# Optimization experiments

Hardware: AMD Instinct MI355X
Metric: run time of the kernel (lower is better)

## Reference

```python
import jax, jax.numpy as jnp
import numpy as np

NH = 4
TEMP = 0.5

def _ln(x, w, b):
    mu = x.mean(-1, keepdims=True)
    var = ((x - mu) ** 2).mean(-1, keepdims=True)
    return (x - mu) / jnp.sqrt(var + 1e-5) * w + b

def _encoder(x, bias, key_pad, layers):
    # pre-LN torch TransformerEncoder, relu FFN, dropout=0
    Wqkv, bqkv, Wo, bo, ln1w, ln1b, ln2w, ln2b, W1, b1, W2, b2 = layers
    B, L, H = x.shape
    d = H // NH
    scale = 1.0 / np.sqrt(d)
    for i in range(Wqkv.shape[0]):
        y = _ln(x, ln1w[i], ln1b[i])
        qkv = y @ Wqkv[i].T + bqkv[i]
        q, k, v = jnp.split(qkv, 3, axis=-1)
        q = q.reshape(B, L, NH, d).transpose(0, 2, 1, 3)
        k = k.reshape(B, L, NH, d).transpose(0, 2, 1, 3)
        v = v.reshape(B, L, NH, d).transpose(0, 2, 1, 3)
        s = jnp.einsum('bhqd,bhkd->bhqk', q, k) * scale
        if bias is not None:
            s = s + bias
        s = s + key_pad[:, None, None, :]
        a = jax.nn.softmax(s, axis=-1)
        o = jnp.einsum('bhqk,bhkd->bhqd', a, v).transpose(0, 2, 1, 3).reshape(B, L, H)
        x = x + o @ Wo[i].T + bo[i]
        y = _ln(x, ln2w[i], ln2b[i])
        x = x + jax.nn.relu(y @ W1[i].T + b1[i]) @ W2[i].T + b2[i]
    return x

def _layer_params(key, nl, H, F, sc=0.05):
    ks = jax.random.split(key, 4)
    return (jax.random.normal(ks[0], (nl, 3 * H, H)) * sc, jnp.zeros((nl, 3 * H)),
            jax.random.normal(ks[1], (nl, H, H)) * sc, jnp.zeros((nl, H)),
            jnp.ones((nl, H)), jnp.zeros((nl, H)), jnp.ones((nl, H)), jnp.zeros((nl, H)),
            jax.random.normal(ks[2], (nl, F, H)) * sc, jnp.zeros((nl, F)),
            jax.random.normal(ks[3], (nl, H, F)) * sc, jnp.zeros((nl, H)))

def setup_inputs():
    key = jax.random.key(0)
    IN, H, ED, F = 64, 128, 16, 256
    G, NPG = 8, 512
    N = G * NPG
    m, k = 4, 16
    T = N
    S = T * m
    EPS = 24
    E_loc = S * EPS
    E = 65536
    ks = jax.random.split(key, 13)
    x = jax.random.normal(ks[0], (N, IN))
    log_probs = -jnp.abs(jax.random.normal(ks[1], (S,)))
    root = jnp.repeat(jnp.arange(T), m)
    base = (root // NPG) * NPG
    rest = base[:, None] + jax.random.randint(ks[2], (S, k - 1), 0, NPG)
    nodes_sampled = jnp.concatenate([root[:, None], rest], axis=1)
    valid = jnp.ones((S * k,), dtype=bool)
    edge_index_sampled = jax.random.randint(ks[3], (2, E_loc), 0, k)
    edge_ptr = jnp.arange(S + 1) * EPS
    ea_flat = jax.random.normal(ks[4], (E_loc, ED))
    src = jax.random.randint(ks[5], (E,), 0, N)
    dst = (src // NPG) * NPG + jax.random.randint(ks[6], (E,), 0, NPG)
    edge_index = jnp.stack([src, dst])
    edge_attr = jax.random.normal(ks[7], (E, ED))
    batch_vec = jnp.arange(N) // NPG
    ptr = jnp.arange(G + 1) * NPG
    d = dict(x=x, log_probs=log_probs, ea_flat=ea_flat, edge_attr=edge_attr,
             init_W=jax.random.normal(ks[8], (H, IN + 2)) * 0.05, init_b=jnp.zeros((H,)),
             loc_ep_W=jax.random.normal(ks[9], (NH, ED)) * 0.05, loc_ep_b=jnp.zeros((NH,)),
             glob_ep_W=jax.random.normal(ks[10], (NH, ED)) * 0.05, glob_ep_b=jnp.zeros((NH,)),
             loc_nw=jnp.ones((H,)), loc_nb=jnp.zeros((H,)),
             glob_nw=jnp.ones((H,)), glob_nb=jnp.zeros((H,)),
             nodes_sampled=nodes_sampled, edge_index_sampled=edge_index_sampled,
             edge_ptr=edge_ptr, edge_index=edge_index, batch_vec=batch_vec,
             ptr=ptr, valid=valid)
    names = ['Wqkv', 'bqkv', 'Wo', 'bo', 'ln1w', 'ln1b', 'ln2w', 'ln2b', 'W1', 'b1', 'W2', 'b2']
    for n, a in zip(names, _layer_params(ks[11], 4, H, F)):
        d['loc_' + n] = a
    for n, a in zip(names, _layer_params(ks[12], 4, H, F)):
        d['glob_' + n] = a
    return d

def reference(x, log_probs, ea_flat, edge_attr, init_W, init_b, loc_ep_W, loc_ep_b,
              glob_ep_W, glob_ep_b, loc_nw, loc_nb, glob_nw, glob_nb,
              loc_Wqkv, loc_bqkv, loc_Wo, loc_bo, loc_ln1w, loc_ln1b, loc_ln2w, loc_ln2b,
              loc_W1, loc_b1, loc_W2, loc_b2,
              glob_Wqkv, glob_bqkv, glob_Wo, glob_bo, glob_ln1w, glob_ln1b, glob_ln2w, glob_ln2b,
              glob_W1, glob_b1, glob_W2, glob_b2,
              nodes_sampled, edge_index_sampled, edge_ptr, edge_index, batch_vec, ptr, valid):
    S, k = nodes_sampled.shape
    N = x.shape[0]
    T = N
    m = S // T
    G = ptr.shape[0] - 1
    max_N = N // G  # equal-size graphs
    H = init_W.shape[0]
    # ---- phase 1: flatten subgraphs + init features ----
    x_flat = x[nodes_sampled.reshape(-1)]                         # [S*k, IN]
    root_global = jnp.repeat(jnp.arange(T), m)                    # [S]
    root_local = jnp.argmax(nodes_sampled == root_global[:, None], axis=1)
    root_mask = jnp.zeros((S * k,), x.dtype).at[jnp.arange(S) * k + root_local].set(1.0)
    lp = jnp.where(jnp.isfinite(log_probs), log_probs, 0.0)
    lp_flat = jnp.repeat(lp, k)[:, None] * valid[:, None].astype(x.dtype)
    h = jnp.concatenate([x_flat, lp_flat, root_mask[:, None]], axis=1) @ init_W.T + init_b
    # ---- local edge bias (scatter-add) ----
    E_loc = ea_flat.shape[0]
    sub = jnp.searchsorted(edge_ptr, jnp.arange(E_loc), side='right') - 1
    eap = ea_flat @ loc_ep_W.T + loc_ep_b                         # [E_loc, NH]
    lbias = jnp.zeros((S, k, k, NH), x.dtype).at[sub, edge_index_sampled[0], edge_index_sampled[1]].add(eap).transpose(0, 3, 1, 2)
    v2 = valid.reshape(S, k)
    key_pad_l = jnp.where(v2, 0.0, -1e9).astype(x.dtype)
    loc_layers = (loc_Wqkv, loc_bqkv, loc_Wo, loc_bo, loc_ln1w, loc_ln1b, loc_ln2w, loc_ln2b, loc_W1, loc_b1, loc_W2, loc_b2)
    out = _encoder(h.reshape(S, k, H), lbias, key_pad_l, loc_layers)
    out = _ln(out, loc_nw, loc_nb)
    vf = v2.astype(x.dtype)[..., None]
    sub_embs = (out * vf).sum(1) / jnp.maximum(vf.sum(1), 1.0)    # [S, H]
    # ---- weighted-mean aggregation over m samples per target node ----
    w = jax.nn.softmax(log_probs.reshape(T, m) / TEMP, axis=1)
    node_embs = jnp.einsum('tm,tmh->th', w, sub_embs.reshape(T, m, H))
    # ---- global phase: to_dense_batch + edge-bias transformer ----
    pos = jnp.arange(N) - ptr[batch_vec]
    dense = jnp.zeros((G, max_N, H), x.dtype).at[batch_vec, pos].set(node_embs)
    vmask = jnp.zeros((G, max_N), bool).at[batch_vec, pos].set(True)
    g = batch_vec[edge_index[0]]
    sl = edge_index[0] - ptr[g]
    dl = edge_index[1] - ptr[g]
    eag = edge_attr @ glob_ep_W.T + glob_ep_b
    gbias = jnp.zeros((G, max_N, max_N, NH), x.dtype).at[g, sl, dl].add(eag).transpose(0, 3, 1, 2)
    key_pad_g = jnp.where(vmask, 0.0, -1e9).astype(x.dtype)
    glob_layers = (glob_Wqkv, glob_bqkv, glob_Wo, glob_bo, glob_ln1w, glob_ln1b, glob_ln2w, glob_ln2b, glob_W1, glob_b1, glob_W2, glob_b2)
    gout = _encoder(dense, gbias, key_pad_g, glob_layers)
    gout = _ln(gout, glob_nw, glob_nb)
    return (gout * vmask[..., None].astype(x.dtype)).sum(1)      # [G, H]
```

## Files before the change

kernel.cpp:

```cpp
#include <hip/hip_runtime.h>
#include <math.h>

#define IN_F      64
#define H_DIM     128
#define NH_       4
#define DH_       32
#define FF_DIM    256
#define KSUB      16
#define S_SEQ     16384
#define E_LOC     393216
#define G_NUM     8
#define NPG_      512
#define N_NODES   4096
#define E_GLOB    65536
#define NLAYERS   4
#define SCALE_ATT 0.17677669529663687f

#define WQKV_SZ   (3*H_DIM*H_DIM)
#define WO_SZ     (H_DIM*H_DIM)
#define W1_SZ     (FF_DIM*H_DIM)
#define W2_SZ     (H_DIM*FF_DIM)

#define ATT(sg)   (4352 + (sg) * 2560)
#define PS_OFF    9472
#define STG_SZ    10112

typedef __bf16 bf16x8 __attribute__((ext_vector_type(8)));
typedef float  f32x4  __attribute__((ext_vector_type(4)));

__device__ __forceinline__ unsigned short f2bf(float f) {
    unsigned u = __float_as_uint(f);
    unsigned r = (u + 0x7fffu + ((u >> 16) & 1u)) >> 16;
    return (unsigned short)r;
}

__device__ __forceinline__ f32x4 mfma16(bf16x8 a, bf16x8 b, f32x4 c) {
    return __builtin_amdgcn_mfma_f32_16x16x32_bf16(a, b, c, 0, 0, 0);
}

__device__ __forceinline__ void ln_to_row(const float (&X)[8][4],
    const float* __restrict__ w, const float* __restrict__ b,
    unsigned short* rowb, int r, int q)
{
    float s1[4] = {0,0,0,0}, s2[4] = {0,0,0,0};
    #pragma unroll
    for (int t = 0; t < 8; ++t)
        #pragma unroll
        for (int i = 0; i < 4; ++i) { float v = X[t][i]; s1[i] += v; s2[i] += v*v; }
    #pragma unroll
    for (int i = 0; i < 4; ++i) {
        float a = s1[i], c = s2[i];
        a += __shfl_xor(a, 1, 16); a += __shfl_xor(a, 2, 16);
        a += __shfl_xor(a, 4, 16); a += __shfl_xor(a, 8, 16);
        c += __shfl_xor(c, 1, 16); c += __shfl_xor(c, 2, 16);
        c += __shfl_xor(c, 4, 16); c += __shfl_xor(c, 8, 16);
        float mu = a * (1.f / H_DIM);
        float var = c * (1.f / H_DIM) - mu * mu;
        s1[i] = mu; s2[i] = rsqrtf(fmaxf(var, 0.f) + 1e-5f);
    }
    for (int t = 0; t < 8; ++t) {
        float wv = w[t * 16 + r], bv = b[t * 16 + r];
        #pragma unroll
        for (int i = 0; i < 4; ++i)
            rowb[(q * 4 + i) * 136 + t * 16 + r] = f2bf((X[t][i] - s1[i]) * s2[i] * wv + bv);
    }
}

__device__ __forceinline__ void ln_mean_out(const float (&X)[8][4],
    const float* __restrict__ fnw, const float* __restrict__ fnb,
    float* __restrict__ dst, int r, int q)
{
    float s1[4] = {0,0,0,0}, s2[4] = {0,0,0,0};
    #pragma unroll
    for (int t = 0; t < 8; ++t)
        #pragma unroll
        for (int i = 0; i < 4; ++i) { float v = X[t][i]; s1[i] += v; s2[i] += v*v; }
    #pragma unroll
    for (int i = 0; i < 4; ++i) {
        float a = s1[i], c = s2[i];
        a += __shfl_xor(a, 1, 16); a += __shfl_xor(a, 2, 16);
        a += __shfl_xor(a, 4, 16); a += __shfl_xor(a, 8, 16);
        c += __shfl_xor(c, 1, 16); c += __shfl_xor(c, 2, 16);
        c += __shfl_xor(c, 4, 16); c += __shfl_xor(c, 8, 16);
        float mu = a * (1.f / H_DIM);
        float var = c * (1.f / H_DIM) - mu * mu;
        s1[i] = mu; s2[i] = rsqrtf(fmaxf(var, 0.f) + 1e-5f);
    }
    float colsum[8];
    #pragma unroll
    for (int t = 0; t < 8; ++t) {
        float wv = fnw[t * 16 + r], bv = fnb[t * 16 + r];
        float cs = 0.f;
        #pragma unroll
        for (int i = 0; i < 4; ++i) cs += (X[t][i] - s1[i]) * s2[i] * wv + bv;
        cs += __shfl_xor(cs, 16, 64);
        cs += __shfl_xor(cs, 32, 64);
        colsum[t] = cs;
    }
    float c0 = (q == 0) ? colsum[0] : (q == 1) ? colsum[1] : (q == 2) ? colsum[2] : colsum[3];
    float c1 = (q == 0) ? colsum[4] : (q == 1) ? colsum[5] : (q == 2) ? colsum[6] : colsum[7];
    dst[q * 16 + r]       = c0 * (1.f / KSUB);
    dst[(q + 4) * 16 + r] = c1 * (1.f / KSUB);
}

__global__ __launch_bounds__(256) void conv_all_k(
    const float* __restrict__ lWqkv, const float* __restrict__ lWo,
    const float* __restrict__ lW1, const float* __restrict__ lW2,
    const float* __restrict__ x,
    const float* __restrict__ gWqkv, const float* __restrict__ gWo,
    const float* __restrict__ gW1, const float* __restrict__ gW2,
    const float* __restrict__ init_W,
    unsigned short* __restrict__ wq_b, unsigned short* __restrict__ wo_b,
    unsigned short* __restrict__ w1_b, unsigned short* __restrict__ w2_b,
    unsigned short* __restrict__ x_b,
    unsigned short* __restrict__ gwq_b, unsigned short* __restrict__ gwo_b,
    unsigned short* __restrict__ gw1_b, unsigned short* __restrict__ gw2_b,
    unsigned short* __restrict__ wi_b)
{
    int b = blockIdx.x, t = threadIdx.x;
    const float* src; unsigned short* dst; int base;
    if (b < 768)       { src = lWqkv; dst = wq_b;  base = b; }
    else if (b < 1024) { src = lWo;   dst = wo_b;  base = b - 768; }
    else if (b < 1536) { src = lW1;   dst = w1_b;  base = b - 1024; }
    else if (b < 2048) { src = lW2;   dst = w2_b;  base = b - 1536; }
    else if (b < 3072) { src = x;     dst = x_b;   base = b - 2048; }
    else if (b < 3840) { src = gWqkv; dst = gwq_b; base = b - 3072; }
    else if (b < 4096) { src = gWo;   dst = gwo_b; base = b - 3840; }
    else if (b < 4608) { src = gW1;   dst = gw1_b; base = b - 4096; }
    else if (b < 5120) { src = gW2;   dst = gw2_b; base = b - 4608; }
    else {
        int i = (b - 5120) * 256 + t;
        int row = i >> 6, c = i & 63;
        wi_b[i] = f2bf(init_W[row * 66 + c]);
        return;
    }
    int i = base * 256 + t;
    dst[i] = f2bf(src[i]);
}

__global__ __launch_bounds__(64) void local_encoder_k(
    const unsigned short* __restrict__ xb16,
    const float* __restrict__ log_probs,
    const float* __restrict__ ea_flat,
    const float* __restrict__ init_W,
    const float* __restrict__ init_b,
    const unsigned short* __restrict__ wi_b,
    const float* __restrict__ ep_W, const float* __restrict__ ep_b,
    const int* __restrict__ nodes, const int* __restrict__ eis,
    const unsigned short* __restrict__ wqb, const unsigned short* __restrict__ wob,
    const unsigned short* __restrict__ w1b, const unsigned short* __restrict__ w2b,
    const float* __restrict__ bqkv, const float* __restrict__ bo,
    const float* __restrict__ ln1w, const float* __restrict__ ln1b,
    const float* __restrict__ ln2w, const float* __restrict__ ln2b,
    const float* __restrict__ b1, const float* __restrict__ b2,
    const float* __restrict__ fnw, const float* __restrict__ fnb,
    float* __restrict__ sub_embs)
{
    __shared__ unsigned short stg[STG_SZ];

    const int lane = threadIdx.x & 63;
    const int r = lane & 15, q = lane >> 4;
    const int s0 = blockIdx.x * 2;
    float* biasWrk = (float*)(stg + 4352);

    {
        float2 z2f; z2f.x = 0.f; z2f.y = 0.f;
        for (int i = lane; i < 1024; i += 64) ((float2*)biasWrk)[i] = z2f;
    }

    int ndA = nodes[s0 * KSUB + r];
    int ndB = nodes[(s0 + 1) * KSUB + r];
    int rootA = s0 >> 2, rootB = (s0 + 1) >> 2;
    unsigned long long balA = __ballot((q == 0) && (ndA == rootA));
    unsigned long long balB = __ballot((q == 0) && (ndB == rootB));
    int rjA = balA ? (__ffsll((long long)balA) - 1) : 0;
    int rjB = balB ? (__ffsll((long long)balB) - 1) : 0;
    float lpA = log_probs[s0];     if (!isfinite(lpA)) lpA = 0.f;
    float lpB = log_probs[s0 + 1]; if (!isfinite(lpB)) lpB = 0.f;

    if (lane < 48) {
        int ls = lane / 24, ee = lane % 24;
        int e = (s0 + ls) * 24 + ee;
        int i0 = eis[e], i1 = eis[E_LOC + e];
        const float* ea = ea_flat + (size_t)e * 16;
        float4 e0 = *(const float4*)(ea), e1 = *(const float4*)(ea + 4);
        float4 e2 = *(const float4*)(ea + 8), e3 = *(const float4*)(ea + 12);
        #pragma unroll
        for (int h = 0; h < NH_; ++h) {
            const float* wp = ep_W + h * 16;
            float v = ep_b[h]
                + e0.x * wp[0]  + e0.y * wp[1]  + e0.z * wp[2]  + e0.w * wp[3]
                + e1.x * wp[4]  + e1.y * wp[5]  + e1.z * wp[6]  + e1.w * wp[7]
                + e2.x * wp[8]  + e2.y * wp[9]  + e2.z * wp[10] + e2.w * wp[11]
                + e3.x * wp[12] + e3.y * wp[13] + e3.z * wp[14] + e3.w * wp[15];
            atomicAdd(&biasWrk[ls * 1024 + (h * 16 + i0) * 16 + i1], v);
        }
    }

    for (int i2 = lane; i2 < 256; i2 += 64) {
        int sg = i2 >> 7, row = (i2 >> 3) & 15, seg = i2 & 7;
        int nd = __shfl(sg ? ndB : ndA, row, 64);
        *(uint4*)(stg + sg * 2176 + row * 136 + seg * 8) =
            *(const uint4*)(xb16 + (size_t)nd * IN_F + seg * 8);
    }

    float bT[2][NH_][4];
    #pragma unroll
    for (int sg = 0; sg < 2; ++sg)
        #pragma unroll
        for (int h = 0; h < NH_; ++h)
            #pragma unroll
            for (int i = 0; i < 4; ++i)
                bT[sg][h][i] = biasWrk[sg * 1024 + (h * 16 + q * 4 + i) * 16 + r];

    {
        uint2 z2; z2.x = 0; z2.y = 0;
        for (int i = lane; i < 320; i += 64) ((uint2*)(stg + ATT(0) + 1280))[i] = z2;
        for (int i = lane; i < 320; i += 64) ((uint2*)(stg + ATT(1) + 1280))[i] = z2;
    }

    float X[2][8][4];
    {
        bf16x8 aA0 = *(const bf16x8*)(stg + r * 136 + q * 8);
        bf16x8 aA1 = *(const bf16x8*)(stg + r * 136 + 32 + q * 8);
        bf16x8 aB0 = *(const bf16x8*)(stg + 2176 + r * 136 + q * 8);
        bf16x8 aB1 = *(const bf16x8*)(stg + 2176 + r * 136 + 32 + q * 8);
        const unsigned short* wr0 = wi_b + (size_t)r * 64 + q * 8;
        bf16x8 c0 = *(const bf16x8*)(wr0);
        bf16x8 c1 = *(const bf16x8*)(wr0 + 32);
        for (int t = 0; t < 8; ++t) {
            bf16x8 n0, n1;
            if (t < 7) {
                const unsigned short* wn = wr0 + (t + 1) * 1024;
                n0 = *(const bf16x8*)(wn);
                n1 = *(const bf16x8*)(wn + 32);
            }
            f32x4 accA = {0.f,0.f,0.f,0.f}, accB = {0.f,0.f,0.f,0.f};
            accA = mfma16(aA0, c0, accA); accA = mfma16(aA1, c1, accA);
            accB = mfma16(aB0, c0, accB); accB = mfma16(aB1, c1, accB);
            int o = t * 16 + r;
            float w64 = init_W[o * 66 + 64], w65 = init_W[o * 66 + 65], bb = init_b[o];
            #pragma unroll
            for (int i = 0; i < 4; ++i) {
                float vA = accA[i] + lpA * w64 + bb;
                float vB = accB[i] + lpB * w64 + bb;
                if (q * 4 + i == rjA) vA += w65;
                if (q * 4 + i == rjB) vB += w65;
                X[0][t][i] = vA; X[1][t][i] = vB;
            }
            c0 = n0; c1 = n1;
        }
    }

    for (int l = 0; l < NLAYERS; ++l) {
        const unsigned short* wq_l = wqb + (size_t)l * WQKV_SZ;
        const unsigned short* wo_l = wob + (size_t)l * WO_SZ;
        const unsigned short* w1_l = w1b + (size_t)l * W1_SZ;
        const unsigned short* w2_l = w2b + (size_t)l * W2_SZ;

        ln_to_row(X[0], ln1w + l * H_DIM, ln1b + l * H_DIM, stg, r, q);
        ln_to_row(X[1], ln1w + l * H_DIM, ln1b + l * H_DIM, stg + 2176, r, q);
        bf16x8 af[2][4];
        #pragma unroll
        for (int sg = 0; sg < 2; ++sg)
            #pragma unroll
            for (int kt = 0; kt < 4; ++kt)
                af[sg][kt] = *(const bf16x8*)(stg + sg * 2176 + r * 136 + kt * 32 + q * 8);

        for (int h = 0; h < NH_; ++h) {
            #pragma unroll
            for (int t = 0; t < 2; ++t) {
                #pragma unroll
                for (int p = 0; p < 3; ++p) {
                    const unsigned short* wr =
                        wq_l + (size_t)(p * H_DIM + h * DH_ + t * 16 + r) * H_DIM + q * 8;
                    bf16x8 c0 = *(const bf16x8*)(wr);
                    bf16x8 c1 = *(const bf16x8*)(wr + 32);
                    bf16x8 c2 = *(const bf16x8*)(wr + 64);
                    bf16x8 c3 = *(const bf16x8*)(wr + 96);
                    f32x4 aA = {0.f,0.f,0.f,0.f}, aB = {0.f,0.f,0.f,0.f};
                    aA = mfma16(af[0][0], c0, aA); aB = mfma16(af[1][0], c0, aB);
                    aA = mfma16(af[0][1], c1, aA); aB = mfma16(af[1][1], c1, aB);
                    aA = mfma16(af[0][2], c2, aA); aB = mfma16(af[1][2], c2, aB);
                    aA = mfma16(af[0][3], c3, aA); aB = mfma16(af[1][3], c3, aB);
                    float bb = bqkv[l * 384 + p * H_DIM + h * DH_ + t * 16 + r];
                    if (p < 2) {
                        int off = p * 640;
                        #pragma unroll
                        for (int i = 0; i < 4; ++i) {
                            stg[ATT(0) + off + (q * 4 + i) * 40 + t * 16 + r] = f2bf(aA[i] + bb);
                            stg[ATT(1) + off + (q * 4 + i) * 40 + t * 16 + r] = f2bf(aB[i] + bb);
                        }
                    } else {
                        unsigned short vA0 = f2bf(aA[0] + bb), vA1 = f2bf(aA[1] + bb);
                        unsigned short vA2 = f2bf(aA[2] + bb), vA3 = f2bf(aA[3] + bb);
                        uint2 pkA; pkA.x = (unsigned)vA0 | ((unsigned)vA1 << 16);
                        pkA.y = (unsigned)vA2 | ((unsigned)vA3 << 16);
                        *(uint2*)(stg + ATT(0) + 1280 + (t * 16 + r) * 40 + q * 4) = pkA;
                        unsigned short vB0 = f2bf(aB[0] + bb), vB1 = f2bf(aB[1] + bb);
                        unsigned short vB2 = f2bf(aB[2] + bb), vB3 = f2bf(aB[3] + bb);
                        uint2 pkB; pkB.x = (unsigned)vB0 | ((unsigned)vB1 << 16);
                        pkB.y = (unsigned)vB2 | ((unsigned)vB3 << 16);
                        *(uint2*)(stg + ATT(1) + 1280 + (t * 16 + r) * 40 + q * 4) = pkB;
                    }
                }
            }
            #pragma unroll
            for (int sg = 0; sg < 2; ++sg) {
                const int ab = ATT(sg);
                bf16x8 aq = *(const bf16x8*)(stg + ab + r * 40 + q * 8);
                bf16x8 bk = *(const bf16x8*)(stg + ab + 640 + r * 40 + q * 8);
                f32x4 sc = mfma16(aq, bk, (f32x4){0.f,0.f,0.f,0.f});
                #pragma unroll
                for (int i = 0; i < 4; ++i) {
                    float v = sc[i] * SCALE_ATT + bT[sg][h][i];
                    float mx = v;
                    mx = fmaxf(mx, __shfl_xor(mx, 1, 16)); mx = fmaxf(mx, __shfl_xor(mx, 2, 16));
                    mx = fmaxf(mx, __shfl_xor(mx, 4, 16)); mx = fmaxf(mx, __shfl_xor(mx, 8, 16));
                    float e = __expf(v - mx);
                    float sum = e;
                    sum += __shfl_xor(sum, 1, 16); sum += __shfl_xor(sum, 2, 16);
                    sum += __shfl_xor(sum, 4, 16); sum += __shfl_xor(sum, 8, 16);
                    float pv = e / sum;
                    stg[PS_OFF + (q * 4 + i) * 40 + r] = f2bf(pv);
                    stg[PS_OFF + (q * 4 + i) * 40 + 16 + r] = 0;
                }
                bf16x8 ap = *(const bf16x8*)(stg + PS_OFF + r * 40 + q * 8);
                #pragma unroll
                for (int t = 0; t < 2; ++t) {
                    bf16x8 bv = *(const bf16x8*)(stg + ab + 1280 + (t * 16 + r) * 40 + q * 8);
                    f32x4 o = mfma16(ap, bv, (f32x4){0.f,0.f,0.f,0.f});
                    #pragma unroll
                    for (int i = 0; i < 4; ++i)
                        stg[sg * 2176 + (q * 4 + i) * 136 + h * DH_ + t * 16 + r] = f2bf(o[i]);
                }
            }
        }

        {
            bf16x8 ao[2][4];
            #pragma unroll
            for (int sg = 0; sg < 2; ++sg)
                #pragma unroll
                for (int kt = 0; kt < 4; ++kt)
                    ao[sg][kt] = *(const bf16x8*)(stg + sg * 2176 + r * 136 + kt * 32 + q * 8);
            const unsigned short* wr0 = wo_l + (size_t)r * H_DIM + q * 8;
            bf16x8 co[4], no[4];
            #pragma unroll
            for (int kt = 0; kt < 4; ++kt) co[kt] = *(const bf16x8*)(wr0 + kt * 32);
            for (int nt = 0; nt < 8; ++nt) {
                if (nt < 7) {
                    const unsigned short* wn = wr0 + (size_t)(nt + 1) * 2048;
                    #pragma unroll
                    for (int kt = 0; kt < 4; ++kt) no[kt] = *(const bf16x8*)(wn + kt * 32);
                }
                f32x4 aA = {0.f,0.f,0.f,0.f}, aB = {0.f,0.f,0.f,0.f};
                #pragma unroll
                for (int kt = 0; kt < 4; ++kt) {
                    aA = mfma16(ao[0][kt], co[kt], aA);
                    aB = mfma16(ao[1][kt], co[kt], aB);
                }
                float bov = bo[l * H_DIM + nt * 16 + r];
                #pragma unroll
                for (int i = 0; i < 4; ++i) {
                    X[0][nt][i] += aA[i] + bov;
                    X[1][nt][i] += aB[i] + bov;
                }
                #pragma unroll
                for (int kt = 0; kt < 4; ++kt) co[kt] = no[kt];
            }
        }

        ln_to_row(X[0], ln2w + l * H_DIM, ln2b + l * H_DIM, stg, r, q);
        ln_to_row(X[1], ln2w + l * H_DIM, ln2b + l * H_DIM, stg + 2176, r, q);

        {
            bf16x8 a2[2][4];
            #pragma unroll
            for (int sg = 0; sg < 2; ++sg)
                #pragma unroll
                for (int kt = 0; kt < 4; ++kt)
                    a2[sg][kt] = *(const bf16x8*)(stg + sg * 2176 + r * 136 + kt * 32 + q * 8);
            const unsigned short* wr0 = w1_l + (size_t)r * H_DIM + q * 8;
            bf16x8 c1b[4], n1b[4];
            #pragma unroll
            for (int kt = 0; kt < 4; ++kt) c1b[kt] = *(const bf16x8*)(wr0 + kt * 32);
            for (int nt = 0; nt < 16; ++nt) {
                if (nt < 15) {
                    const unsigned short* wn = wr0 + (size_t)(nt + 1) * 2048;
                    #pragma unroll
                    for (int kt = 0; kt < 4; ++kt) n1b[kt] = *(const bf16x8*)(wn + kt * 32);
                }
                float b1v = b1[l * FF_DIM + nt * 16 + r];
                #pragma unroll
                for (int sg = 0; sg < 2; ++sg) {
                    f32x4 acc = {0.f,0.f,0.f,0.f};
                    #pragma unroll
                    for (int kt = 0; kt < 4; ++kt) acc = mfma16(a2[sg][kt], c1b[kt], acc);
                    #pragma unroll
                    for (int i = 0; i < 4; ++i)
                        stg[sg * 4224 + (q * 4 + i) * 264 + nt * 16 + r] =
                            f2bf(fmaxf(acc[i] + b1v, 0.f));
                }
                #pragma unroll
                for (int kt = 0; kt < 4; ++kt) c1b[kt] = n1b[kt];
            }
            for (int kp = 0; kp < 2; ++kp) {
                bf16x8 a1[2][4];
                #pragma unroll
                for (int sg = 0; sg < 2; ++sg)
                    #pragma unroll
                    for (int kt = 0; kt < 4; ++kt)
                        a1[sg][kt] = *(const bf16x8*)(stg + sg * 4224 + r * 264 + kp * 128 + kt * 32 + q * 8);
                const unsigned short* wr2 = w2_l + (size_t)r * FF_DIM + kp * 128 + q * 8;
                bf16x8 c2b[4], n2b[4];
                #pragma unroll
                for (int kt = 0; kt < 4; ++kt) c2b[kt] = *(const bf16x8*)(wr2 + kt * 32);
                for (int nt = 0; nt < 8; ++nt) {
                    if (nt < 7) {
                        const unsigned short* wn = wr2 + (size_t)(nt + 1) * 4096;
                        #pragma unroll
                        for (int kt = 0; kt < 4; ++kt) n2b[kt] = *(const bf16x8*)(wn + kt * 32);
                    }
                    f32x4 aA = {0.f,0.f,0.f,0.f}, aB = {0.f,0.f,0.f,0.f};
                    #pragma unroll
                    for (int kt = 0; kt < 4; ++kt) {
                        aA = mfma16(a1[0][kt], c2b[kt], aA);
                        aB = mfma16(a1[1][kt], c2b[kt], aB);
                    }
                    float b2v = (kp == 0) ? b2[l * H_DIM + nt * 16 + r] : 0.f;
                    #pragma unroll
                    for (int i = 0; i < 4; ++i) {
                        X[0][nt][i] += aA[i] + b2v;
                        X[1][nt][i] += aB[i] + b2v;
                    }
                    #pragma unroll
                    for (int kt = 0; kt < 4; ++kt) c2b[kt] = n2b[kt];
                }
            }
        }
    }

    ln_mean_out(X[0], fnw, fnb, sub_embs + (size_t)s0 * H_DIM, r, q);
    ln_mean_out(X[1], fnw, fnb, sub_embs + (size_t)(s0 + 1) * H_DIM, r, q);
}

__global__ __launch_bounds__(256) void aggregate_k(const float* __restrict__ sub,
    const float* __restrict__ lp, const int* __restrict__ bvec,
    const int* __restrict__ ptrg, float* __restrict__ xg)
{
    int idx = blockIdx.x * 256 + threadIdx.x;
    int t = idx >> 7, i = idx & 127;
    float l0 = lp[t * 4 + 0] * 2.f, l1 = lp[t * 4 + 1] * 2.f;
    float l2 = lp[t * 4 + 2] * 2.f, l3 = lp[t * 4 + 3] * 2.f;
    float mx = fmaxf(fmaxf(l0, l1), fmaxf(l2, l3));
    float e0 = __expf(l0 - mx), e1 = __expf(l1 - mx);
    float e2 = __expf(l2 - mx), e3 = __expf(l3 - mx);
    float inv = 1.f / (e0 + e1 + e2 + e3);
    float v = e0 * sub[((size_t)t * 4 + 0) * H_DIM + i]
            + e1 * sub[((size_t)t * 4 + 1) * H_DIM + i]
            + e2 * sub[((size_t)t * 4 + 2) * H_DIM + i]
            + e3 * sub[((size_t)t * 4 + 3) * H_DIM + i];
    int g = bvec[t];
    int pos = t - ptrg[g];
    xg[((size_t)(g * NPG_ + pos)) * H_DIM + i] = v * inv;
}

__global__ __launch_bounds__(256) void zero_k(float4* __restrict__ p)
{
    p[(size_t)blockIdx.x * 256 + threadIdx.x] = make_float4(0.f, 0.f, 0.f, 0.f);
}

__global__ __launch_bounds__(256) void gbias_scatter_k(
    const float* __restrict__ edge_attr, const int* __restrict__ eidx,
    const int* __restrict__ bvec, const int* __restrict__ ptrg,
    const float* __restrict__ epW, const float* __restrict__ epb,
    float* __restrict__ gbias)
{
    int e = blockIdx.x * 256 + threadIdx.x;
    int src = eidx[e], dst = eidx[E_GLOB + e];
    int g = bvec[src];
    int sl = src - ptrg[g], dl = dst - ptrg[g];
    const float* ea = edge_attr + (size_t)e * 16;
    #pragma unroll
    for (int h = 0; h < NH_; ++h) {
        float v = epb[h];
        #pragma unroll
        for (int t = 0; t < 16; ++t) v += ea[t] * epW[h * 16 + t];
        atomicAdd(&gbias[(((size_t)g * NH_ + h) * NPG_ + sl) * NPG_ + dl], v);
    }
}

__global__ __launch_bounds__(256) void ln_rows_bf_k(const float* __restrict__ xin,
    const float* __restrict__ w, const float* __restrict__ b,
    unsigned short* __restrict__ yout)
{
    int row = blockIdx.x * 16 + (threadIdx.x >> 4);
    int t = threadIdx.x & 15;
    const float* xr = xin + (size_t)row * H_DIM;
    float s1 = 0.f, s2 = 0.f;
    for (int i = t; i < H_DIM; i += 16) { float v = xr[i]; s1 += v; s2 += v * v; }
    for (int m2 = 8; m2 >= 1; m2 >>= 1) {
        s1 += __shfl_xor(s1, m2, 16);
        s2 += __shfl_xor(s2, m2, 16);
    }
    float mu  = s1 * (1.f / H_DIM);
    float var = s2 * (1.f / H_DIM) - mu * mu;
    float rs  = rsqrtf(fmaxf(var, 0.f) + 1e-5f);
    unsigned short* yr = yout + (size_t)row * H_DIM;
    for (int i = t; i < H_DIM; i += 16) yr[i] = f2bf((xr[i] - mu) * rs * w[i] + b[i]);
}

__global__ __launch_bounds__(256) void softmax_bf_k(float* __restrict__ sc)
{
    int row = blockIdx.x * 4 + (threadIdx.x >> 6);
    int lane = threadIdx.x & 63;
    float4* r4 = (float4*)(sc + (size_t)row * NPG_);
    float4 v0 = r4[lane * 2], v1 = r4[lane * 2 + 1];
    float mx = fmaxf(fmaxf(fmaxf(v0.x, v0.y), fmaxf(v0.z, v0.w)),
                     fmaxf(fmaxf(v1.x, v1.y), fmaxf(v1.z, v1.w)));
    for (int m2 = 32; m2 >= 1; m2 >>= 1) mx = fmaxf(mx, __shfl_xor(mx, m2, 64));
    v0.x = __expf(v0.x - mx); v0.y = __expf(v0.y - mx);
    v0.z = __expf(v0.z - mx); v0.w = __expf(v0.w - mx);
    v1.x = __expf(v1.x - mx); v1.y = __expf(v1.y - mx);
    v1.z = __expf(v1.z - mx); v1.w = __expf(v1.w - mx);
    float s = v0.x + v0.y + v0.z + v0.w + v1.x + v1.y + v1.z + v1.w;
    for (int m2 = 32; m2 >= 1; m2 >>= 1) s += __shfl_xor(s, m2, 64);
// ... 145 lines not shown
    dim3 grid((N + 63) / 64, M / 64, Z);
    hipLaunchKernelGGL(gemm_mfma_k, grid, dim3(256), 0, st, A, B, C, bias, D, vt,
        M, N, K, lda, ldb, ldc, ldd, sAg, sAh, sBg, sBh, sCg, sCh, sDg, sDh, alpha, op);
}

extern "C" void kernel_launch(void* const* d_in, const int* in_sizes, int n_in,
                              void* d_out, int out_size, void* d_ws, size_t ws_size,
                              hipStream_t stream)
{
    const float* x         = (const float*)d_in[0];
    const float* lp        = (const float*)d_in[1];
    const float* ea_flat   = (const float*)d_in[2];
    const float* edge_attr = (const float*)d_in[3];
    const float* init_W    = (const float*)d_in[4];
    const float* init_b    = (const float*)d_in[5];
    const float* lepW      = (const float*)d_in[6];
    const float* lepb      = (const float*)d_in[7];
    const float* gepW      = (const float*)d_in[8];
    const float* gepb      = (const float*)d_in[9];
    const float* lnw       = (const float*)d_in[10];
    const float* lnb       = (const float*)d_in[11];
    const float* gnw       = (const float*)d_in[12];
    const float* gnb       = (const float*)d_in[13];
    const int*   nodes     = (const int*)d_in[14];
    const int*   eis       = (const int*)d_in[15];
    const int*   eptr      = (const int*)d_in[16];  (void)eptr;
    const int*   eidx      = (const int*)d_in[17];
    const int*   bvec      = (const int*)d_in[18];
    const int*   ptrg      = (const int*)d_in[19];
    const float* lWqkv = (const float*)d_in[21];
    const float* lbqkv = (const float*)d_in[22];
    const float* lWo   = (const float*)d_in[23];
    const float* lbo   = (const float*)d_in[24];
    const float* lln1w = (const float*)d_in[25];
    const float* lln1b = (const float*)d_in[26];
    const float* lln2w = (const float*)d_in[27];
    const float* lln2b = (const float*)d_in[28];
    const float* lW1   = (const float*)d_in[29];
    const float* lb1   = (const float*)d_in[30];
    const float* lW2   = (const float*)d_in[31];
    const float* lb2   = (const float*)d_in[32];
    const float* gWqkv = (const float*)d_in[33];
    const float* gbqkv = (const float*)d_in[34];
    const float* gWo   = (const float*)d_in[35];
    const float* gbo   = (const float*)d_in[36];
    const float* gln1w = (const float*)d_in[37];
    const float* gln1b = (const float*)d_in[38];
    const float* gln2w = (const float*)d_in[39];
    const float* gln2b = (const float*)d_in[40];
    const float* gW1   = (const float*)d_in[41];
    const float* gb1   = (const float*)d_in[42];
    const float* gW2   = (const float*)d_in[43];
    const float* gb2   = (const float*)d_in[44];

    float* out = (float*)d_out;
    float* ws  = (float*)d_ws;
    float* gbias   = ws;
    float* scores  = ws + 8388608;
    float* subembs = scores;
    float* xg      = ws + 16777216;
    unsigned short* qkvg_b = (unsigned short*)(ws + 17301504);
    unsigned short* yg_b   = (unsigned short*)(ws + 18087936);
    unsigned short* attg_b = (unsigned short*)(ws + 18350080);
    unsigned short* ffg_b  = (unsigned short*)(ws + 18612224);
    unsigned short* vt_b   = (unsigned short*)(ws + 19136512);
    unsigned short* gw     = (unsigned short*)(ws + 19398656);

    unsigned short* wb   = (unsigned short*)gbias;
    unsigned short* wq_b = wb;
    unsigned short* wo_b = wb + 196608;
    unsigned short* w1_b = wb + 262144;
    unsigned short* w2_b = wb + 393216;
    unsigned short* x_b  = wb + 524288;
    unsigned short* wi_b = wb + 786432;
    unsigned short* gwq_b = gw;
    unsigned short* gwo_b = gw + 196608;
    unsigned short* gw1_b = gw + 262144;
    unsigned short* gw2_b = gw + 393216;

    hipLaunchKernelGGL(conv_all_k, dim3(5152), dim3(256), 0, stream,
        lWqkv, lWo, lW1, lW2, x, gWqkv, gWo, gW1, gW2, init_W,
        wq_b, wo_b, w1_b, w2_b, x_b, gwq_b, gwo_b, gw1_b, gw2_b, wi_b);

    hipLaunchKernelGGL(local_encoder_k, dim3(S_SEQ / 2), dim3(64), 0, stream,
        x_b, lp, ea_flat, init_W, init_b, wi_b, lepW, lepb, nodes, eis,
        wq_b, wo_b, w1_b, w2_b,
        lbqkv, lbo, lln1w, lln1b, lln2w, lln2b, lb1, lb2,
        lnw, lnb, subembs);

    hipLaunchKernelGGL(aggregate_k, dim3(2048), dim3(256), 0, stream,
        subembs, lp, bvec, ptrg, xg);

    hipLaunchKernelGGL(zero_k, dim3(8192), dim3(256), 0, stream, (float4*)gbias);
    hipLaunchKernelGGL(gbias_scatter_k, dim3(E_GLOB / 256), dim3(256), 0, stream,
        edge_attr, eidx, bvec, ptrg, gepW, gepb, gbias);

    hipLaunchKernelGGL(ln_rows_bf_k, dim3(256), dim3(256), 0, stream,
        xg, gln1w, gln1b, yg_b);

    for (int l = 0; l < NLAYERS; ++l) {
        launch_gmm(stream, yg_b, gwq_b + (size_t)l * WQKV_SZ, qkvg_b,
                   gbqkv + l * 384, nullptr, vt_b, 4096, 384, 128, 128, 128, 384, 0,
                   0, 0, 0, 0, 0, 0, 0, 0, 1.f, 4, 1);
        launch_gmm(stream, qkvg_b, qkvg_b + 128, scores, nullptr, gbias, nullptr,
                   512, 512, 32, 384, 384, 512, 512,
                   (long)512 * 384, 32, (long)512 * 384, 32,
                   1048576, 262144, 1048576, 262144, SCALE_ATT, 1, 32);
        hipLaunchKernelGGL(softmax_bf_k, dim3(4096), dim3(256), 0, stream, scores);
        launch_gmm(stream, (const unsigned short*)scores, vt_b, attg_b,
                   nullptr, nullptr, nullptr, 512, 32, 512, 1024, 512, 128, 0,
                   2097152, 524288, 65536, 16384, 65536, 32, 0, 0, 1.f, 0, 32);
        hipLaunchKernelGGL(gemm_ln_k<4>, dim3(256), dim3(64), 0, stream,
            attg_b, gwo_b + (size_t)l * WO_SZ, gbo + l * H_DIM, xg,
            gln2w + l * H_DIM, gln2b + l * H_DIM, (void*)yg_b, 0);
        launch_gmm(stream, yg_b, gw1_b + (size_t)l * W1_SZ, ffg_b,
                   gb1 + l * FF_DIM, nullptr, nullptr, 4096, 256, 128, 128, 128, 256, 0,
                   0, 0, 0, 0, 0, 0, 0, 0, 1.f, 3, 1);
        const float* nw = (l < 3) ? (gln1w + (l + 1) * H_DIM) : gnw;
        const float* nb = (l < 3) ? (gln1b + (l + 1) * H_DIM) : gnb;
        void* yo = (l < 3) ? (void*)yg_b : (void*)scores;
        hipLaunchKernelGGL(gemm_ln_k<8>, dim3(256), dim3(64), 0, stream,
            ffg_b, gw2_b + (size_t)l * W2_SZ, gb2 + l * H_DIM, xg,
            nw, nb, yo, (l < 3) ? 0 : 1);
    }

    hipLaunchKernelGGL(reduce_out_k, dim3(G_NUM), dim3(128), 0, stream, scores, out);
}
```

Before: 1.571 ms.

## Process one subgraph per wavefront in local encoder to cut registers and LDS

The local encoder kernel now handles a single 16-node subgraph per 64-thread block instead of two, halving register arrays (X, fragments) and shrinking shared memory from about 20KB to about 9.5KB. It adds a min-blocks-per-CU hint and doubles the grid to cover every sequence. The aim is higher occupancy to hide global weight-load latency. In exchange, each weight fragment loaded from global or L2 now feeds one MFMA instead of two, so weight traffic per subgraph doubles.

```diff
diff --git a/kernel.cpp b/kernel.cpp
--- a/kernel.cpp
+++ b/kernel.cpp
@@ -21,9 +21,10 @@
 #define W1_SZ     (FF_DIM*H_DIM)
 #define W2_SZ     (H_DIM*FF_DIM)
 
-#define ATT(sg)   (4352 + (sg) * 2560)
-#define PS_OFF    9472
-#define STG_SZ    10112
+#define QS_B      2176
+#define KS_B      2816
+#define VT_B      3456
+#define STG_SZ    4736
 
 typedef __bf16 bf16x8 __attribute__((ext_vector_type(8)));
 typedef float  f32x4  __attribute__((ext_vector_type(4)));
@@ -138,7 +139,7 @@
     dst[i] = f2bf(src[i]);
 }
 
-__global__ __launch_bounds__(64) void local_encoder_k(
+__global__ __launch_bounds__(64, 4) void local_encoder_k(
     const unsigned short* __restrict__ xb16,
     const float* __restrict__ log_probs,
     const float* __restrict__ ea_flat,
@@ -160,27 +161,22 @@
 
     const int lane = threadIdx.x & 63;
     const int r = lane & 15, q = lane >> 4;
-    const int s0 = blockIdx.x * 2;
-    float* biasWrk = (float*)(stg + 4352);
+    const int s = blockIdx.x;
+    float* biasWrk = (float*)(stg + QS_B);
 
     {
         float2 z2f; z2f.x = 0.f; z2f.y = 0.f;
-        for (int i = lane; i < 1024; i += 64) ((float2*)biasWrk)[i] = z2f;
-    }
-
-    int ndA = nodes[s0 * KSUB + r];
-    int ndB = nodes[(s0 + 1) * KSUB + r];
-    int rootA = s0 >> 2, rootB = (s0 + 1) >> 2;
-    unsigned long long balA = __ballot((q == 0) && (ndA == rootA));
-    unsigned long long balB = __ballot((q == 0) && (ndB == rootB));
-    int rjA = balA ? (__ffsll((long long)balA) - 1) : 0;
-    int rjB = balB ? (__ffsll((long long)balB) - 1) : 0;
-    float lpA = log_probs[s0];     if (!isfinite(lpA)) lpA = 0.f;
-    float lpB = log_probs[s0 + 1]; if (!isfinite(lpB)) lpB = 0.f;
-
-    if (lane < 48) {
-        int ls = lane / 24, ee = lane % 24;
-        int e = (s0 + ls) * 24 + ee;
+        for (int i = lane; i < 512; i += 64) ((float2*)biasWrk)[i] = z2f;
+    }
+
+    int nd = nodes[s * KSUB + r];
+    int root = s >> 2;
+    unsigned long long bal = __ballot((q == 0) && (nd == root));
+    int rj = bal ? (__ffsll((long long)bal) - 1) : 0;
+    float lp = log_probs[s]; if (!isfinite(lp)) lp = 0.f;
+
+    if (lane < 24) {
+        int e = s * 24 + lane;
         int i0 = eis[e], i1 = eis[E_LOC + e];
         const float* ea = ea_flat + (size_t)e * 16;
         float4 e0 = *(const float4*)(ea), e1 = *(const float4*)(ea + 4);
@@ -193,38 +189,28 @@
                 + e1.x * wp[4]  + e1.y * wp[5]  + e1.z * wp[6]  + e1.w * wp[7]
                 + e2.x * wp[8]  + e2.y * wp[9]  + e2.z * wp[10] + e2.w * wp[11]
                 + e3.x * wp[12] + e3.y * wp[13] + e3.z * wp[14] + e3.w * wp[15];
-            atomicAdd(&biasWrk[ls * 1024 + (h * 16 + i0) * 16 + i1], v);
-        }
-    }
-
-    for (int i2 = lane; i2 < 256; i2 += 64) {
-        int sg = i2 >> 7, row = (i2 >> 3) & 15, seg = i2 & 7;
-        int nd = __shfl(sg ? ndB : ndA, row, 64);
-        *(uint4*)(stg + sg * 2176 + row * 136 + seg * 8) =
-            *(const uint4*)(xb16 + (size_t)nd * IN_F + seg * 8);
-    }
-
-    float bT[2][NH_][4];
-    #pragma unroll
-    for (int sg = 0; sg < 2; ++sg)
-        #pragma unroll
-        for (int h = 0; h < NH_; ++h)
-            #pragma unroll
-            for (int i = 0; i < 4; ++i)
-                bT[sg][h][i] = biasWrk[sg * 1024 + (h * 16 + q * 4 + i) * 16 + r];
-
+            atomicAdd(&biasWrk[(h * 16 + i0) * 16 + i1], v);
+        }
+    }
+
+    for (int i2 = lane; i2 < 128; i2 += 64) {
+        int row = i2 >> 3, seg = i2 & 7;
+        int ndr = __shfl(nd, row, 64);
+        *(uint4*)(stg + row * 136 + seg * 8) =
+            *(const uint4*)(xb16 + (size_t)ndr * IN_F + seg * 8);
+    }
+
+    float bT[NH_][4];
+    #pragma unroll
+    for (int h = 0; h < NH_; ++h)
+        #pragma unroll
+        for (int i = 0; i < 4; ++i)
+            bT[h][i] = biasWrk[(h * 16 + q * 4 + i) * 16 + r];
+
+    float X[8][4];
     {
-        uint2 z2; z2.x = 0; z2.y = 0;
-        for (int i = lane; i < 320; i += 64) ((uint2*)(stg + ATT(0) + 1280))[i] = z2;
-        for (int i = lane; i < 320; i += 64) ((uint2*)(stg + ATT(1) + 1280))[i] = z2;
-    }
-
-    float X[2][8][4];
-    {
-        bf16x8 aA0 = *(const bf16x8*)(stg + r * 136 + q * 8);
-        bf16x8 aA1 = *(const bf16x8*)(stg + r * 136 + 32 + q * 8);
-        bf16x8 aB0 = *(const bf16x8*)(stg + 2176 + r * 136 + q * 8);
-        bf16x8 aB1 = *(const bf16x8*)(stg + 2176 + r * 136 + 32 + q * 8);
+        bf16x8 a0 = *(const bf16x8*)(stg + r * 136 + q * 8);
+        bf16x8 a1 = *(const bf16x8*)(stg + r * 136 + 32 + q * 8);
         const unsigned short* wr0 = wi_b + (size_t)r * 64 + q * 8;
         bf16x8 c0 = *(const bf16x8*)(wr0);
         bf16x8 c1 = *(const bf16x8*)(wr0 + 32);
@@ -235,18 +221,15 @@
                 n0 = *(const bf16x8*)(wn);
                 n1 = *(const bf16x8*)(wn + 32);
             }
-            f32x4 accA = {0.f,0.f,0.f,0.f}, accB = {0.f,0.f,0.f,0.f};
-            accA = mfma16(aA0, c0, accA); accA = mfma16(aA1, c1, accA);
-            accB = mfma16(aB0, c0, accB); accB = mfma16(aB1, c1, accB);
+            f32x4 acc = {0.f,0.f,0.f,0.f};
+            acc = mfma16(a0, c0, acc); acc = mfma16(a1, c1, acc);
             int o = t * 16 + r;
             float w64 = init_W[o * 66 + 64], w65 = init_W[o * 66 + 65], bb = init_b[o];
             #pragma unroll
             for (int i = 0; i < 4; ++i) {
-                float vA = accA[i] + lpA * w64 + bb;
-                float vB = accB[i] + lpB * w64 + bb;
-                if (q * 4 + i == rjA) vA += w65;
-                if (q * 4 + i == rjB) vB += w65;
-                X[0][t][i] = vA; X[1][t][i] = vB;
+                float v = acc[i] + lp * w64 + bb;
+                if (q * 4 + i == rj) v += w65;
+                X[t][i] = v;
             }
             c0 = n0; c1 = n1;
         }
@@ -258,14 +241,17 @@
         const unsigned short* w1_l = w1b + (size_t)l * W1_SZ;
         const unsigned short* w2_l = w2b + (size_t)l * W2_SZ;
 
-        ln_to_row(X[0], ln1w + l * H_DIM, ln1b + l * H_DIM, stg, r, q);
-        ln_to_row(X[1], ln1w + l * H_DIM, ln1b + l * H_DIM, stg + 2176, r, q);
-        bf16x8 af[2][4];
-        #pragma unroll
-        for (int sg = 0; sg < 2; ++sg)
-            #pragma unroll
-            for (int kt = 0; kt < 4; ++kt)
-                af[sg][kt] = *(const bf16x8*)(stg + sg * 2176 + r * 136 + kt * 32 + q * 8);
+        ln_to_row(X, ln1w + l * H_DIM, ln1b + l * H_DIM, stg, r, q);
+
+        {
+            uint4 z4; z4.x = 0; z4.y = 0; z4.z = 0; z4.w = 0;
+            *(uint4*)(stg + VT_B + (lane >> 1) * 40 + 16 + (lane & 1) * 8) = z4;
+        }
+
+        bf16x8 af[4];
+        #pragma unroll
+        for (int kt = 0; kt < 4; ++kt)
+            af[kt] = *(const bf16x8*)(stg + r * 136 + kt * 32 + q * 8);
 
         for (int h = 0; h < NH_; ++h) {
             #pragma unroll
@@ -278,72 +264,59 @@
                     bf16x8 c1 = *(const bf16x8*)(wr + 32);
                     bf16x8 c2 = *(const bf16x8*)(wr + 64);
                     bf16x8 c3 = *(const bf16x8*)(wr + 96);
-                    f32x4 aA = {0.f,0.f,0.f,0.f}, aB = {0.f,0.f,0.f,0.f};
-                    aA = mfma16(af[0][0], c0, aA); aB = mfma16(af[1][0], c0, aB);
-                    aA = mfma16(af[0][1], c1, aA); aB = mfma16(af[1][1], c1, aB);
-                    aA = mfma16(af[0][2], c2, aA); aB = mfma16(af[1][2], c2, aB);
-                    aA = mfma16(af[0][3], c3, aA); aB = mfma16(af[1][3], c3, aB);
+                    f32x4 a = {0.f,0.f,0.f,0.f};
+                    a = mfma16(af[0], c0, a);
+                    a = mfma16(af[1], c1, a);
+                    a = mfma16(af[2], c2, a);
+                    a = mfma16(af[3], c3, a);
                     float bb = bqkv[l * 384 + p * H_DIM + h * DH_ + t * 16 + r];
                     if (p < 2) {
-                        int off = p * 640;
+                        int off = QS_B + p * 640;
                         #pragma unroll
-                        for (int i = 0; i < 4; ++i) {
-                            stg[ATT(0) + off + (q * 4 + i) * 40 + t * 16 + r] = f2bf(aA[i] + bb);
-                            stg[ATT(1) + off + (q * 4 + i) * 40 + t * 16 + r] = f2bf(aB[i] + bb);
-                        }
+                        for (int i = 0; i < 4; ++i)
+                            stg[off + (q * 4 + i) * 40 + t * 16 + r] = f2bf(a[i] + bb);
                     } else {
-                        unsigned short vA0 = f2bf(aA[0] + bb), vA1 = f2bf(aA[1] + bb);
-                        unsigned short vA2 = f2bf(aA[2] + bb), vA3 = f2bf(aA[3] + bb);
-                        uint2 pkA; pkA.x = (unsigned)vA0 | ((unsigned)vA1 << 16);
-                        pkA.y = (unsigned)vA2 | ((unsigned)vA3 << 16);
-                        *(uint2*)(stg + ATT(0) + 1280 + (t * 16 + r) * 40 + q * 4) = pkA;
-                        unsigned short vB0 = f2bf(aB[0] + bb), vB1 = f2bf(aB[1] + bb);
-                        unsigned short vB2 = f2bf(aB[2] + bb), vB3 = f2bf(aB[3] + bb);
-                        uint2 pkB; pkB.x = (unsigned)vB0 | ((unsigned)vB1 << 16);
-                        pkB.y = (unsigned)vB2 | ((unsigned)vB3 << 16);
-                        *(uint2*)(stg + ATT(1) + 1280 + (t * 16 + r) * 40 + q * 4) = pkB;
+                        unsigned short v0 = f2bf(a[0] + bb), v1 = f2bf(a[1] + bb);
+                        unsigned short v2 = f2bf(a[2] + bb), v3 = f2bf(a[3] + bb);
+                        uint2 pk; pk.x = (unsigned)v0 | ((unsigned)v1 << 16);
+                        pk.y = (unsigned)v2 | ((unsigned)v3 << 16);
+                        *(uint2*)(stg + VT_B + (t * 16 + r) * 40 + q * 4) = pk;
                     }
                 }
             }
+            bf16x8 aq = *(const bf16x8*)(stg + QS_B + r * 40 + q * 8);
+            bf16x8 bk = *(const bf16x8*)(stg + KS_B + r * 40 + q * 8);
+            f32x4 sc = mfma16(aq, bk, (f32x4){0.f,0.f,0.f,0.f});
             #pragma unroll
-            for (int sg = 0; sg < 2; ++sg) {
-                const int ab = ATT(sg);
-                bf16x8 aq = *(const bf16x8*)(stg + ab + r * 40 + q * 8);
-                bf16x8 bk = *(const bf16x8*)(stg + ab + 640 + r * 40 + q * 8);
-                f32x4 sc = mfma16(aq, bk, (f32x4){0.f,0.f,0.f,0.f});
-                #pragma unroll
-                for (int i = 0; i < 4; ++i) {
-                    float v = sc[i] * SCALE_ATT + bT[sg][h][i];
-                    float mx = v;
-                    mx = fmaxf(mx, __shfl_xor(mx, 1, 16)); mx = fmaxf(mx, __shfl_xor(mx, 2, 16));
-                    mx = fmaxf(mx, __shfl_xor(mx, 4, 16)); mx = fmaxf(mx, __shfl_xor(mx, 8, 16));
-                    float e = __expf(v - mx);
-                    float sum = e;
-                    sum += __shfl_xor(sum, 1, 16); sum += __shfl_xor(sum, 2, 16);
-                    sum += __shfl_xor(sum, 4, 16); sum += __shfl_xor(sum, 8, 16);
-                    float pv = e / sum;
-                    stg[PS_OFF + (q * 4 + i) * 40 + r] = f2bf(pv);
-                    stg[PS_OFF + (q * 4 + i) * 40 + 16 + r] = 0;
-                }
-                bf16x8 ap = *(const bf16x8*)(stg + PS_OFF + r * 40 + q * 8);
-                #pragma unroll
-                for (int t = 0; t < 2; ++t) {
-                    bf16x8 bv = *(const bf16x8*)(stg + ab + 1280 + (t * 16 + r) * 40 + q * 8);
-                    f32x4 o = mfma16(ap, bv, (f32x4){0.f,0.f,0.f,0.f});
-                    #pragma unroll
-                    for (int i = 0; i < 4; ++i)
-                        stg[sg * 2176 + (q * 4 + i) * 136 + h * DH_ + t * 16 + r] = f2bf(o[i]);
-                }
+            for (int i = 0; i < 4; ++i) {
+                float v = sc[i] * SCALE_ATT + bT[h][i];
+                float mx = v;
+                mx = fmaxf(mx, __shfl_xor(mx, 1, 16)); mx = fmaxf(mx, __shfl_xor(mx, 2, 16));
+                mx = fmaxf(mx, __shfl_xor(mx, 4, 16)); mx = fmaxf(mx, __shfl_xor(mx, 8, 16));
+                float e = __expf(v - mx);
+                float sum = e;
+                sum += __shfl_xor(sum, 1, 16); sum += __shfl_xor(sum, 2, 16);
+                sum += __shfl_xor(sum, 4, 16); sum += __shfl_xor(sum, 8, 16);
+                float pv = e / sum;
+                stg[QS_B + (q * 4 + i) * 40 + r] = f2bf(pv);
+                stg[QS_B + (q * 4 + i) * 40 + 16 + r] = 0;
+            }
+            bf16x8 ap = *(const bf16x8*)(stg + QS_B + r * 40 + q * 8);
+            #pragma unroll
+            for (int t = 0; t < 2; ++t) {
+                bf16x8 bv = *(const bf16x8*)(stg + VT_B + (t * 16 + r) * 40 + q * 8);
+                f32x4 o = mfma16(ap, bv, (f32x4){0.f,0.f,0.f,0.f});
+                #pragma unroll
+                for (int i = 0; i < 4; ++i)
+                    stg[(q * 4 + i) * 136 + h * DH_ + t * 16 + r] = f2bf(o[i]);
             }
         }
 
         {
-            bf16x8 ao[2][4];
+            bf16x8 ao[4];
             #pragma unroll
-            for (int sg = 0; sg < 2; ++sg)
-                #pragma unroll
-                for (int kt = 0; kt < 4; ++kt)
-                    ao[sg][kt] = *(const bf16x8*)(stg + sg * 2176 + r * 136 + kt * 32 + q * 8);
+            for (int kt = 0; kt < 4; ++kt)
+                ao[kt] = *(const bf16x8*)(stg + r * 136 + kt * 32 + q * 8);
             const unsigned short* wr0 = wo_l + (size_t)r * H_DIM + q * 8;
             bf16x8 co[4], no[4];
             #pragma unroll
@@ -354,33 +327,24 @@
                     #pragma unroll
                     for (int kt = 0; kt < 4; ++kt) no[kt] = *(const bf16x8*)(wn + kt * 32);
                 }
-                f32x4 aA = {0.f,0.f,0.f,0.f}, aB = {0.f,0.f,0.f,0.f};
-                #pragma unroll
-                for (int kt = 0; kt < 4; ++kt) {
-                    aA = mfma16(ao[0][kt], co[kt], aA);
-                    aB = mfma16(ao[1][kt], co[kt], aB);
-                }
+                f32x4 a = {0.f,0.f,0.f,0.f};
+                #pragma unroll
+                for (int kt = 0; kt < 4; ++kt) a = mfma16(ao[kt], co[kt], a);
                 float bov = bo[l * H_DIM + nt * 16 + r];
                 #pragma unroll
-                for (int i = 0; i < 4; ++i) {
-                    X[0][nt][i] += aA[i] + bov;
-                    X[1][nt][i] += aB[i] + bov;
-                }
+                for (int i = 0; i < 4; ++i) X[nt][i] += a[i] + bov;
                 #pragma unroll
                 for (int kt = 0; kt < 4; ++kt) co[kt] = no[kt];
             }
         }
 
-        ln_to_row(X[0], ln2w + l * H_DIM, ln2b + l * H_DIM, stg, r, q);
-        ln_to_row(X[1], ln2w + l * H_DIM, ln2b + l * H_DIM, stg + 2176, r, q);
+        ln_to_row(X, ln2w + l * H_DIM, ln2b + l * H_DIM, stg, r, q);
 
         {
-            bf16x8 a2[2][4];
+            bf16x8 a2[4];
             #pragma unroll
-            for (int sg = 0; sg < 2; ++sg)
-                #pragma unroll
-                for (int kt = 0; kt < 4; ++kt)
-                    a2[sg][kt] = *(const bf16x8*)(stg + sg * 2176 + r * 136 + kt * 32 + q * 8);
+            for (int kt = 0; kt < 4; ++kt)
+                a2[kt] = *(const bf16x8*)(stg + r * 136 + kt * 32 + q * 8);
             const unsigned short* wr0 = w1_l + (size_t)r * H_DIM + q * 8;
             bf16x8 c1b[4], n1b[4];
             #pragma unroll
@@ -392,26 +356,20 @@
                     for (int kt = 0; kt < 4; ++kt) n1b[kt] = *(const bf16x8*)(wn + kt * 32);
                 }
                 float b1v = b1[l * FF_DIM + nt * 16 + r];
-                #pragma unroll
-                for (int sg = 0; sg < 2; ++sg) {
-                    f32x4 acc = {0.f,0.f,0.f,0.f};
-                    #pragma unroll
-                    for (int kt = 0; kt < 4; ++kt) acc = mfma16(a2[sg][kt], c1b[kt], acc);
-                    #pragma unroll
-                    for (int i = 0; i < 4; ++i)
-                        stg[sg * 4224 + (q * 4 + i) * 264 + nt * 16 + r] =
-                            f2bf(fmaxf(acc[i] + b1v, 0.f));
-                }
+                f32x4 acc = {0.f,0.f,0.f,0.f};
+                #pragma unroll
+                for (int kt = 0; kt < 4; ++kt) acc = mfma16(a2[kt], c1b[kt], acc);
+                #pragma unroll
+                for (int i = 0; i < 4; ++i)
+                    stg[(q * 4 + i) * 264 + nt * 16 + r] = f2bf(fmaxf(acc[i] + b1v, 0.f));
                 #pragma unroll
                 for (int kt = 0; kt < 4; ++kt) c1b[kt] = n1b[kt];
             }
             for (int kp = 0; kp < 2; ++kp) {
-                bf16x8 a1[2][4];
-                #pragma unroll
-                for (int sg = 0; sg < 2; ++sg)
-                    #pragma unroll
-                    for (int kt = 0; kt < 4; ++kt)
-                        a1[sg][kt] = *(const bf16x8*)(stg + sg * 4224 + r * 264 + kp * 128 + kt * 32 + q * 8);
+                bf16x8 a1[4];
+                #pragma unroll
+                for (int kt = 0; kt < 4; ++kt)
+                    a1[kt] = *(const bf16x8*)(stg + r * 264 + kp * 128 + kt * 32 + q * 8);
                 const unsigned short* wr2 = w2_l + (size_t)r * FF_DIM + kp * 128 + q * 8;
                 bf16x8 c2b[4], n2b[4];
                 #pragma unroll
@@ -422,18 +380,12 @@
                         #pragma unroll
                         for (int kt = 0; kt < 4; ++kt) n2b[kt] = *(const bf16x8*)(wn + kt * 32);
                     }
-                    f32x4 aA = {0.f,0.f,0.f,0.f}, aB = {0.f,0.f,0.f,0.f};
+                    f32x4 a = {0.f,0.f,0.f,0.f};
                     #pragma unroll
-                    for (int kt = 0; kt < 4; ++kt) {
-                        aA = mfma16(a1[0][kt], c2b[kt], aA);
-                        aB = mfma16(a1[1][kt], c2b[kt], aB);
-                    }
+                    for (int kt = 0; kt < 4; ++kt) a = mfma16(a1[kt], c2b[kt], a);
                     float b2v = (kp == 0) ? b2[l * H_DIM + nt * 16 + r] : 0.f;
                     #pragma unroll
-                    for (int i = 0; i < 4; ++i) {
-                        X[0][nt][i] += aA[i] + b2v;
-                        X[1][nt][i] += aB[i] + b2v;
-                    }
+                    for (int i = 0; i < 4; ++i) X[nt][i] += a[i] + b2v;
                     #pragma unroll
                     for (int kt = 0; kt < 4; ++kt) c2b[kt] = n2b[kt];
                 }
@@ -441,8 +393,7 @@
         }
     }
 
-    ln_mean_out(X[0], fnw, fnb, sub_embs + (size_t)s0 * H_DIM, r, q);
-    ln_mean_out(X[1], fnw, fnb, sub_embs + (size_t)(s0 + 1) * H_DIM, r, q);
+    ln_mean_out(X, fnw, fnb, sub_embs + (size_t)s * H_DIM, r, q);
 }
 
 __global__ __launch_bounds__(256) void aggregate_k(const float* __restrict__ sub,
@@ -754,7 +705,7 @@
         lWqkv, lWo, lW1, lW2, x, gWqkv, gWo, gW1, gW2, init_W,
         wq_b, wo_b, w1_b, w2_b, x_b, gwq_b, gwo_b, gw1_b, gw2_b, wi_b);
 
-    hipLaunchKernelGGL(local_encoder_k, dim3(S_SEQ / 2), dim3(64), 0, stream,
+    hipLaunchKernelGGL(local_encoder_k, dim3(S_SEQ), dim3(64), 0, stream,
         x_b, lp, ea_flat, init_W, init_b, wi_b, lepW, lepb, nodes, eis,
         wq_b, wo_b, w1_b, w2_b,
         lbqkv, lbo, lln1w, lln1b, lln2w, lln2b, lb1, lb2,
```

Measured after the change: 2.559 ms. +62.9%, slower.
